# Kernel tuning notes

Measured on AMD Instinct MI355X. Metric: run time of the kernel, lower is better.

Reference implementation:

```python
import jax, jax.numpy as jnp
import numpy as np
import math

NUM_GROUPS = 8
NUM_HEADS = 4
EPS = 1e-5


def group_norm(x, gamma, beta):
    B, C, H, W = x.shape
    g = x.reshape(B, NUM_GROUPS, C // NUM_GROUPS, H, W)
    mean = g.mean(axis=(2, 3, 4), keepdims=True)
    var = g.var(axis=(2, 3, 4), keepdims=True)
    g = (g - mean) * jax.lax.rsqrt(var + EPS)
    x = g.reshape(B, C, H, W)
    return x * gamma[None, :, None, None] + beta[None, :, None, None]


def setup_inputs() -> dict:
    key = jax.random.key(0)
    ks = jax.random.split(key, 4)
    B, C, H, W = 4, 256, 64, 64
    x = jax.random.normal(ks[0], (B, C, H, W), dtype=jnp.float32)
    gamma = jnp.ones((C,), dtype=jnp.float32)
    beta = jnp.zeros((C,), dtype=jnp.float32)
    w_qkv = jax.random.normal(ks[1], (3 * C, C), dtype=jnp.float32) / math.sqrt(C)
    b_qkv = jnp.zeros((3 * C,), dtype=jnp.float32)
    w_proj = jax.random.normal(ks[2], (C, C), dtype=jnp.float32) / math.sqrt(C)
    b_proj = jnp.zeros((C,), dtype=jnp.float32)
    return {"x": x, "gamma": gamma, "beta": beta, "w_qkv": w_qkv,
            "b_qkv": b_qkv, "w_proj": w_proj, "b_proj": b_proj}


def reference(x, gamma, beta, w_qkv, b_qkv, w_proj, b_proj):
    B, C, H, W = x.shape
    hd = C // NUM_HEADS  # head dim
    h = group_norm(x, gamma, beta)
    # 1x1 conv == per-pixel matmul: [B,3C,H,W]
    qkv = jnp.einsum('bchw,oc->bohw', h, w_qkv) + b_qkv[None, :, None, None]
    q, k, v = jnp.split(qkv, 3, axis=1)

    def shape(t):
        # [B,C,H,W] -> [B, heads, HW, hd]
        return t.reshape(B, NUM_HEADS, hd, H * W).transpose(0, 1, 3, 2)

    q, k, v = shape(q), shape(k), shape(v)
    attn = jnp.einsum('bhqd,bhkd->bhqk', q, k) * (1.0 / math.sqrt(hd))
    attn = jax.nn.softmax(attn, axis=-1)
    out = jnp.einsum('bhqk,bhkd->bhqd', attn, v)
    # [B, heads, HW, hd] -> [B, C, H, W]
    out = out.transpose(0, 1, 3, 2).reshape(B, C, H, W)
    out = jnp.einsum('bchw,oc->bohw', out, w_proj) + b_proj[None, :, None, None]
    return x + out
```

## Files before the change

kernel.cpp:

```cpp
#include <hip/hip_runtime.h>
#include <math.h>

#define NB 4
#define C_ 256
#define NG 8
#define CPG 32
#define HW 4096
#define NH 4
#define HD 64
#define EPS 1e-5f
#define QSCALE 0.1803368801111204f

typedef __attribute__((ext_vector_type(8))) short bf16x8_t;
typedef __attribute__((ext_vector_type(4))) float f32x4_t;
typedef const __attribute__((address_space(1))) void g_void;
typedef __attribute__((address_space(3))) void l_void;

__device__ __forceinline__ unsigned short f2bf(float f) {
    unsigned u = __float_as_uint(f);
    u += 0x7FFFu + ((u >> 16) & 1u);
    return (unsigned short)(u >> 16);
}

__device__ __forceinline__ unsigned cvtpk(float lo, float hi) {
    unsigned r;
    asm("v_cvt_pk_bf16_f32 %0, %1, %2" : "=v"(r) : "v"(lo), "v"(hi));
    return r;
}

__device__ __forceinline__ void plswap16(unsigned &a, unsigned &b) {
#if __has_builtin(__builtin_amdgcn_permlane16_swap)
    auto r = __builtin_amdgcn_permlane16_swap(a, b, false, false);
    a = r[0]; b = r[1];
#else
    unsigned as = (unsigned)__shfl_xor((int)a, 16);
    unsigned bs = (unsigned)__shfl_xor((int)b, 16);
    bool hi = (threadIdx.x & 16) != 0;
    unsigned na = hi ? bs : a;
    unsigned nb = hi ? b : as;
    a = na; b = nb;
#endif
}
__device__ __forceinline__ void plswap32(unsigned &a, unsigned &b) {
#if __has_builtin(__builtin_amdgcn_permlane32_swap)
    auto r = __builtin_amdgcn_permlane32_swap(a, b, false, false);
    a = r[0]; b = r[1];
#else
    unsigned as = (unsigned)__shfl_xor((int)a, 32);
    unsigned bs = (unsigned)__shfl_xor((int)b, 32);
    bool hi = (threadIdx.x & 32) != 0;
    unsigned na = hi ? bs : a;
    unsigned nb = hi ? b : as;
    a = na; b = nb;
#endif
}

__global__ __launch_bounds__(256) void gn_stats_wconv_k(const float* __restrict__ x,
                                                        float2* __restrict__ part,
                                                        const float* __restrict__ wq,
                                                        const float* __restrict__ wp,
                                                        unsigned short* __restrict__ wt,
                                                        unsigned short* __restrict__ wpt) {
    if (blockIdx.x >= 1024) {
        int i4 = (blockIdx.x - 1024) * 256 + threadIdx.x;
        const float* src;
        unsigned short* dst;
        int off;
        if (i4 < 49152) { src = wq; dst = wt; off = i4 * 4; }
        else            { src = wp; dst = wpt; off = (i4 - 49152) * 4; }
        float4 v = *(const float4*)(src + off);
        ushort4 o;
        o.x = f2bf(v.x); o.y = f2bf(v.y); o.z = f2bf(v.z); o.w = f2bf(v.w);
        *(ushort4*)(dst + off) = o;
        return;
    }
    int bg = blockIdx.x >> 5, ch = blockIdx.x & 31;
    const float4* base = (const float4*)(x + (size_t)bg * CPG * HW + ch * 4096);
    float s = 0.f, ss = 0.f;
    #pragma unroll
    for (int i = threadIdx.x; i < 1024; i += 256) {
        float4 v = base[i];
        s  += v.x + v.y + v.z + v.w;
        ss += v.x*v.x + v.y*v.y + v.z*v.z + v.w*v.w;
    }
    #pragma unroll
    for (int off = 32; off > 0; off >>= 1) {
        s  += __shfl_down(s, off);
        ss += __shfl_down(ss, off);
    }
    __shared__ float rs[4], rss[4];
    int wv = threadIdx.x >> 6;
    if ((threadIdx.x & 63) == 0) { rs[wv] = s; rss[wv] = ss; }
    __syncthreads();
    if (threadIdx.x == 0)
        part[blockIdx.x] = make_float2(rs[0]+rs[1]+rs[2]+rs[3], rss[0]+rss[1]+rss[2]+rss[3]);
}

__global__ __launch_bounds__(256) void gn_apply_t_k(const float* __restrict__ x,
                                                    const float* __restrict__ gamma,
                                                    const float* __restrict__ beta,
                                                    const float2* __restrict__ part,
                                                    unsigned short* __restrict__ ht) {
    __shared__ unsigned short T[64 * 66];
    __shared__ float sstat[4];
    int b = blockIdx.z, c0 = blockIdx.y * 64, p0 = blockIdx.x * 64;
    int t = threadIdx.x;
    if (t < 64) {
        int half = t >> 5;
        int g = b * NG + (c0 >> 5) + half;
        float2 v = part[g * 32 + (t & 31)];
        float s = v.x, ss = v.y;
        #pragma unroll
        for (int off = 16; off > 0; off >>= 1) {
            s  += __shfl_xor(s, off);
            ss += __shfl_xor(ss, off);
        }
        if ((t & 31) == 0) {
            const float inv = 1.f / (float)(CPG * HW);
            float mean = s * inv;
            float var  = ss * inv - mean * mean;
            sstat[half * 2]     = mean;
            sstat[half * 2 + 1] = rsqrtf(var + EPS);
        }
    }
    __syncthreads();
    int cr = t >> 4, pc = t & 15;
    #pragma unroll
    for (int cp = 0; cp < 4; cp++) {
        int c = c0 + cp * 16 + cr;
        int gl = (cp * 16 + cr) >> 5;
        float mean = sstat[gl * 2], rstd = sstat[gl * 2 + 1];
        float sc = gamma[c] * rstd;
        float sh = beta[c] - mean * sc;
        float4 v = *(const float4*)(x + ((size_t)(b * C_ + c)) * HW + p0 + pc * 4);
        int cc = cp * 16 + cr;
        T[(pc*4 + 0) * 66 + cc] = f2bf(v.x*sc + sh);
        T[(pc*4 + 1) * 66 + cc] = f2bf(v.y*sc + sh);
        T[(pc*4 + 2) * 66 + cc] = f2bf(v.z*sc + sh);
        T[(pc*4 + 3) * 66 + cc] = f2bf(v.w*sc + sh);
    }
    __syncthreads();
    int p = t >> 2, cq = t & 3;
    const unsigned* rp = (const unsigned*)(T + p * 66 + cq * 16);
    unsigned short* dst = ht + ((size_t)b * HW + p0 + p) * 256 + c0 + cq * 16;
    *(uint4*)dst       = make_uint4(rp[0], rp[1], rp[2], rp[3]);
    *(uint4*)(dst + 8) = make_uint4(rp[4], rp[5], rp[6], rp[7]);
}

__global__ __launch_bounds__(256) void gemm_qkv_mfma_k(const unsigned short* __restrict__ wt,
                                                       const unsigned short* __restrict__ ht,
                                                       const float* __restrict__ bias,
                                                       unsigned short* __restrict__ qt,
                                                       unsigned short* __restrict__ kt,
                                                       unsigned short* __restrict__ vv) {
    __shared__ __align__(16) unsigned short smem[24576];
    int t = threadIdx.x, wave = t >> 6, lane = t & 63, quad = lane >> 4, l16 = lane & 15;
    int mq = wave & 1, pq = wave >> 1;
    int L = blockIdx.x;
    int W = (L & 7) * 96 + (L >> 3);
    int b = W / 192;
    int rem = W - b * 192;
    int px = rem / 6;
    int my = rem - px * 6;
    const char* Ag = (const char*)(wt + (size_t)(my * 128) * 256);
    const char* Bg = (const char*)(ht + ((size_t)b * HW + px * 128) * 256);

    int soff[2], lbs[2];
    #pragma unroll
    for (int n = 0; n < 2; n++) {
        int s = n * 256 + t;
        int row = s >> 2, c = (s & 3) ^ (row & 3);
        soff[n] = row * 512 + c * 16;
        lbs[n]  = s * 8;
    }

    auto STAGE = [&](int kc, int buf) {
        const char* a  = Ag + kc * 64;
        const char* bb = Bg + kc * 64;
        #pragma unroll
        for (int n = 0; n < 2; n++) {
            __builtin_amdgcn_global_load_lds((g_void*)(a  + soff[n]), (l_void*)(smem + buf * 8192 + lbs[n]), 16, 0, 0);
            __builtin_amdgcn_global_load_lds((g_void*)(bb + soff[n]), (l_void*)(smem + buf * 8192 + 4096 + lbs[n]), 16, 0, 0);
        }
    };

    f32x4_t acc[4][4];
    const f32x4_t zz = {0.f, 0.f, 0.f, 0.f};
    #pragma unroll
    for (int i = 0; i < 4; i++)
        #pragma unroll
        for (int j = 0; j < 4; j++) acc[i][j] = zz;

    STAGE(0, 0);
    STAGE(1, 1);
    int cur = 0;
    for (int kc = 0; kc < 8; kc++) {
        if (kc < 7) asm volatile("s_waitcnt vmcnt(4)" ::: "memory");
        else        asm volatile("s_waitcnt vmcnt(0)" ::: "memory");
        asm volatile("s_barrier" ::: "memory");
        if (kc + 2 < 8) { int nb = cur + 2; if (nb >= 3) nb -= 3; STAGE(kc + 2, nb); }
        const unsigned short* Ac = smem + cur * 8192;
        const unsigned short* Bc = smem + cur * 8192 + 4096;
        bf16x8_t af[4], bfr[4];
        #pragma unroll
        for (int mi = 0; mi < 4; mi++) {
            int R = mq * 64 + mi * 16 + l16;
            af[mi] = *(const bf16x8_t*)&Ac[(R * 4 + (quad ^ (R & 3))) * 8];
        }
        #pragma unroll
        for (int pi = 0; pi < 4; pi++) {
            int P = pq * 64 + pi * 16 + l16;
            bfr[pi] = *(const bf16x8_t*)&Bc[(P * 4 + (quad ^ (P & 3))) * 8];
        }
        __builtin_amdgcn_s_setprio(1);
        #pragma unroll
        for (int mi = 0; mi < 4; mi++)
            #pragma unroll
            for (int pi = 0; pi < 4; pi++)
                acc[mi][pi] = __builtin_amdgcn_mfma_f32_16x16x32_bf16(af[mi], bfr[pi], acc[mi][pi], 0, 0, 0);
        __builtin_amdgcn_s_setprio(0);
        cur = (cur + 1 == 3) ? 0 : cur + 1;
    }

    int sec = my >> 1;
    int hh = ((my & 1) << 1) | mq;
    if (sec < 2) {
        float scl = (sec == 0) ? QSCALE : 1.f;
        unsigned short* dst = ((sec == 0) ? qt : kt) + (size_t)(b * NH + hh) * HW * 64;
        #pragma unroll
        for (int mi = 0; mi < 4; mi++) {
            int d0 = mi * 16 + quad * 4;
            int mg = my * 128 + mq * 64 + d0;
            #pragma unroll
            for (int pi = 0; pi < 4; pi++) {
                int p = px * 128 + pq * 64 + pi * 16 + l16;
                unsigned lo = cvtpk((acc[mi][pi][0] + bias[mg + 0]) * scl,
                                    (acc[mi][pi][1] + bias[mg + 1]) * scl);
                unsigned hi = cvtpk((acc[mi][pi][2] + bias[mg + 2]) * scl,
                                    (acc[mi][pi][3] + bias[mg + 3]) * scl);
                *(uint2*)(dst + (size_t)p * 64 + d0) = make_uint2(lo, hi);
            }
        }
    } else {
        __syncthreads();
        unsigned short* T = smem;
        #pragma unroll
        for (int mi = 0; mi < 4; mi++) {
            int dT = mq * 64 + mi * 16 + quad * 4;
            int mg = my * 128 + dT;
            #pragma unroll
            for (int pi = 0; pi < 4; pi++) {
                int pl = pq * 64 + pi * 16 + l16;
                #pragma unroll
                for (int r = 0; r < 4; r++)
                    T[(dT + r) * 130 + pl] = f2bf(acc[mi][pi][r] + bias[mg + r]);
            }
        }
        __syncthreads();
        int dT = t >> 1, half = t & 1;
        const unsigned* rp = (const unsigned*)(T + dT * 130 + half * 64);
        unsigned short* dd = vv + ((size_t)(b * 256 + (my & 1) * 128 + dT)) * HW + px * 128 + half * 64;
        #pragma unroll
        for (int q8 = 0; q8 < 8; q8++)
            *(uint4*)(dd + q8 * 8) = make_uint4(rp[q8*4+0], rp[q8*4+1], rp[q8*4+2], rp[q8*4+3]);
    }
}

__global__ __launch_bounds__(256) void gemm_proj_mfma_k(const unsigned short* __restrict__ wpt,
                                                        const unsigned short* __restrict__ ao,
                                                        const float* __restrict__ bias,
                                                        const float* __restrict__ x,
                                                        float* __restrict__ out) {
    int b = blockIdx.z, my = blockIdx.y, px = blockIdx.x;
    int t = threadIdx.x, wave = t >> 6, lane = t & 63, quad = lane >> 4, l16 = lane & 15;
    int mw = wave & 1, pw = wave >> 1;
    const unsigned short* Ab = wpt + (size_t)(my * 64 + mw * 32) * 256;
    const unsigned short* Bb = ao + ((size_t)b * HW + px * 64 + pw * 32) * 256;
    f32x4_t acc[2][2];
    const f32x4_t zz = {0.f, 0.f, 0.f, 0.f};
    acc[0][0] = zz; acc[0][1] = zz; acc[1][0] = zz; acc[1][1] = zz;
    #pragma unroll
    for (int kc = 0; kc < 8; kc++) {
        bf16x8_t af[2], bfr[2];
        #pragma unroll
        for (int mi = 0; mi < 2; mi++)
            af[mi] = *(const bf16x8_t*)(Ab + (mi*16 + l16) * 256 + kc*32 + quad*8);
        #pragma unroll
        for (int pi = 0; pi < 2; pi++)
            bfr[pi] = *(const bf16x8_t*)(Bb + (size_t)(pi*16 + l16) * 256 + kc*32 + quad*8);
        #pragma unroll
        for (int mi = 0; mi < 2; mi++)
            #pragma unroll
            for (int pi = 0; pi < 2; pi++)
                acc[mi][pi] = __builtin_amdgcn_mfma_f32_16x16x32_bf16(af[mi], bfr[pi], acc[mi][pi], 0, 0, 0);
    }
    #pragma unroll
    for (int mi = 0; mi < 2; mi++)
        #pragma unroll
        for (int pi = 0; pi < 2; pi++) {
            int p = px*64 + pw*32 + pi*16 + l16;
            #pragma unroll
            for (int r = 0; r < 4; r++) {
                int m = my*64 + mw*32 + mi*16 + quad*4 + r;
                size_t off = (size_t)(b * C_ + m) * HW + p;
                out[off] = acc[mi][pi][r] + bias[m] + x[off];
            }
        }
}

__global__ __launch_bounds__(512) __attribute__((amdgpu_waves_per_eu(2, 8)))
void attn_k(const unsigned short* __restrict__ qt,
            const unsigned short* __restrict__ kt,
            const unsigned short* __restrict__ vv,
            unsigned short* __restrict__ ao) {
    __shared__ __align__(16) unsigned short smem[24576];
    int t = threadIdx.x;
    int wave = t >> 6, lane = t & 63, quad = lane >> 4, l16 = lane & 15;
    int iw = wave & 3, jw = wave >> 2;
    int L = blockIdx.x;
    int W = (L & 7) * 64 + (L >> 3);
    int i0 = (W & 31) * 128;
    int hh = (W >> 5) & 3;
    int b  = W >> 7;
    const unsigned short* qb = qt + (size_t)(b * NH + hh) * HW * 64;
    const char* kbp = (const char*)(kt + (size_t)(b * NH + hh) * HW * 64);
    const char* vbp = (const char*)(vv + (size_t)(b * NH + hh) * 64 * HW);

    bf16x8_t qf[2][2];
    #pragma unroll
    for (int mi = 0; mi < 2; mi++)
        #pragma unroll
        for (int kc = 0; kc < 2; kc++)
            qf[mi][kc] = *(const bf16x8_t*)(qb + (size_t)(i0 + iw * 32 + mi * 16 + l16) * 64 + kc * 32 + quad * 8);

    f32x4_t oacc[4][2], osum[2];
    const f32x4_t zz = {0.f, 0.f, 0.f, 0.f};
    #pragma unroll
    for (int dt = 0; dt < 4; dt++) { oacc[dt][0] = zz; oacc[dt][1] = zz; }
    osum[0] = zz; osum[1] = zz;

    bf16x8_t ones;
    #pragma unroll
    for (int e = 0; e < 8; e++) ones[e] = (short)0x3F80;

    bool isK = (jw == 0);
    int soff[2], lbase[2];
    #pragma unroll
    for (int n = 0; n < 2; n++) {
        int s = (iw * 2 + n) * 64 + lane;
        int row = s >> 3;
        int c = (s & 7) ^ (row & 7);
        soff[n] = isK ? (row * 128 + c * 16) : (row * (HW * 2) + c * 16);
        lbase[n] = (isK ? 0 : 12288) + (iw * 2 + n) * 512;
    }
    const char* gsrc0 = isK ? kbp : vbp;
    int tstride = isK ? 8192 : 128;

    auto STAGE = [&](int tile, int buf) {
        const char* g = gsrc0 + (size_t)tile * tstride;
        #pragma unroll
        for (int n = 0; n < 2; n++)
            __builtin_amdgcn_global_load_lds((g_void*)(g + soff[n]),
                                             (l_void*)(smem + buf * 4096 + lbase[n]), 16, 0, 0);
    };

    STAGE(0, 0);
    STAGE(1, 1);

    int cur = 0;
    for (int jt = 0; jt < 64; jt++) {
        if (jt < 63) asm volatile("s_waitcnt vmcnt(2)" ::: "memory");
        else         asm volatile("s_waitcnt vmcnt(0)" ::: "memory");
        asm volatile("s_barrier" ::: "memory");
        if (jt + 2 < 64) {
            int nb = cur + 2; if (nb >= 3) nb -= 3;
            STAGE(jt + 2, nb);
        }
        const unsigned short* Kc = smem + cur * 4096;
        const unsigned short* Vc = smem + 12288 + cur * 4096;

        f32x4_t sacc[2][2];
        sacc[0][0] = zz; sacc[0][1] = zz; sacc[1][0] = zz; sacc[1][1] = zz;
        __builtin_amdgcn_s_setprio(1);
        #pragma unroll
        for (int nj = 0; nj < 2; nj++) {
            int j = jw * 32 + nj * 16 + l16;
            int rb = j * 8;
            bf16x8_t kf0 = *(const bf16x8_t*)&Kc[(rb + ((quad    ) ^ (j & 7))) * 8];
            bf16x8_t kf1 = *(const bf16x8_t*)&Kc[(rb + ((4 + quad) ^ (j & 7))) * 8];
            #pragma unroll
            for (int mi = 0; mi < 2; mi++) {
                sacc[mi][nj] = __builtin_amdgcn_mfma_f32_16x16x32_bf16(kf0, qf[mi][0], sacc[mi][nj], 0, 0, 0);
                sacc[mi][nj] = __builtin_amdgcn_mfma_f32_16x16x32_bf16(kf1, qf[mi][1], sacc[mi][nj], 0, 0, 0);
            }
        }
        __builtin_amdgcn_s_setprio(0);

        bf16x8_t pf[2];
        #pragma unroll
        for (int mi = 0; mi < 2; mi++) {
            #pragma unroll
            for (int nj = 0; nj < 2; nj++)
                #pragma unroll
                for (int r = 0; r < 4; r++)
                    sacc[mi][nj][r] = __builtin_amdgcn_exp2f(sacc[mi][nj][r]);

            unsigned lo0 = cvtpk(sacc[mi][0][0], sacc[mi][0][1]);
            unsigned hi0 = cvtpk(sacc[mi][0][2], sacc[mi][0][3]);
            unsigned lo1 = cvtpk(sacc[mi][1][0], sacc[mi][1][1]);
            unsigned hi1 = cvtpk(sacc[mi][1][2], sacc[mi][1][3]);
            plswap32(lo0, lo1); plswap16(lo0, lo1);
            plswap32(hi0, hi1); plswap16(hi0, hi1);
            union { unsigned u[4]; bf16x8_t v8; } pu;
            pu.u[0] = lo0; pu.u[1] = hi0; pu.u[2] = lo1; pu.u[3] = hi1;
            pf[mi] = pu.v8;
        }

        __builtin_amdgcn_s_setprio(1);
        #pragma unroll
        for (int dt = 0; dt < 4; dt++) {
            int d = dt * 16 + l16;
            bf16x8_t vf = *(const bf16x8_t*)&Vc[(d * 8 + ((jw * 4 + quad) ^ (d & 7))) * 8];
            oacc[dt][0] = __builtin_amdgcn_mfma_f32_16x16x32_bf16(vf, pf[0], oacc[dt][0], 0, 0, 0);
            oacc[dt][1] = __builtin_amdgcn_mfma_f32_16x16x32_bf16(vf, pf[1], oacc[dt][1], 0, 0, 0);
        }
        osum[0] = __builtin_amdgcn_mfma_f32_16x16x32_bf16(ones, pf[0], osum[0], 0, 0, 0);
        osum[1] = __builtin_amdgcn_mfma_f32_16x16x32_bf16(ones, pf[1], osum[1], 0, 0, 0);
        __builtin_amdgcn_s_setprio(0);

        cur = (cur + 1 == 3) ? 0 : cur + 1;
    }

    __syncthreads();
    float* Obuf = (float*)smem;
    if (jw == 1) {
        #pragma unroll
        for (int mi = 0; mi < 2; mi++) {
            int R = iw * 32 + mi * 16 + l16;
            #pragma unroll
            for (int dt = 0; dt < 4; dt++)
                *(f32x4_t*)&Obuf[R * 68 + dt * 16 + quad * 4] = oacc[dt][mi];
            if (quad == 0)
                Obuf[R * 68 + 64] = osum[mi][0];
        }
    }
    __syncthreads();
    if (jw == 0) {
        #pragma unroll
        for (int mi = 0; mi < 2; mi++) {
            int R = iw * 32 + mi * 16 + l16;
            float l  = osum[mi][0] + Obuf[R * 68 + 64];
            float c0 = 1.f / l;
            unsigned short* dst = ao + ((size_t)b * HW + i0 + R) * 256 + hh * 64 + quad * 4;
            #pragma unroll
            for (int dt = 0; dt < 4; dt++) {
                f32x4_t o1 = *(const f32x4_t*)&Obuf[R * 68 + dt * 16 + quad * 4];
                unsigned w0 = cvtpk((oacc[dt][mi][0] + o1[0]) * c0,
                                    (oacc[dt][mi][1] + o1[1]) * c0);
                unsigned w1 = cvtpk((oacc[dt][mi][2] + o1[2]) * c0,
                                    (oacc[dt][mi][3] + o1[3]) * c0);
                *(uint2*)(dst + dt * 16) = make_uint2(w0, w1);
            }
        }
    }
}

extern "C" void kernel_launch(void* const* d_in, const int* in_sizes, int n_in,
                              void* d_out, int out_size, void* d_ws, size_t ws_size,
                              hipStream_t stream) {
    const float* x      = (const float*)d_in[0];
    const float* gamma  = (const float*)d_in[1];
    const float* beta   = (const float*)d_in[2];
    const float* w_qkv  = (const float*)d_in[3];
    const float* b_qkv  = (const float*)d_in[4];
    const float* w_proj = (const float*)d_in[5];
    const float* b_proj = (const float*)d_in[6];
    float* out = (float*)d_out;

    float* stats = (float*)d_ws;
    float2* part = (float2*)(stats + 256);
    unsigned short* ht  = (unsigned short*)(stats + 256 + 2048);
    unsigned short* qt  = ht + (size_t)4194304;
    unsigned short* kt  = qt + (size_t)4194304;
    unsigned short* vv  = kt + (size_t)4194304;
    unsigned short* ao  = vv + (size_t)4194304;
    unsigned short* wt  = ao + (size_t)4194304;
    unsigned short* wpt = wt + 196608;

    gn_stats_wconv_k<<<1280, 256, 0, stream>>>(x, part, w_qkv, w_proj, wt, wpt);
    gn_apply_t_k<<<dim3(64, 4, NB), 256, 0, stream>>>(x, gamma, beta, part, ht);
    gemm_qkv_mfma_k<<<768, 256, 0, stream>>>(wt, ht, b_qkv, qt, kt, vv);
    attn_k<<<512, 512, 0, stream>>>(qt, kt, vv, ao);
    gemm_proj_mfma_k<<<dim3(64, 4, NB), 256, 0, stream>>>(wpt, ao, b_proj, x, out);
}
```

Baseline: 190.5 us.

## Stage projection GEMM tiles through LDS with async triple buffering

The output projection GEMM now uses larger 128x128 tiles per block. Operands are staged into swizzled LDS through async global_load_lds with a three-buffer pipeline, replacing direct per-wave global fragment loads. The grid is flattened to 256 blocks with an interleaved block-to-tile mapping, and MFMA priority is raised during compute. This aims to improve operand reuse and overlap loads with MFMA, at the cost of fewer blocks and more LDS per block.

Result: faster. 182.2 us (median of 2 runs) (-4.4%).

```diff
diff --git a/kernel.cpp b/kernel.cpp
--- a/kernel.cpp
+++ b/kernel.cpp
@@ -271,37 +271,83 @@
                                                         const float* __restrict__ bias,
                                                         const float* __restrict__ x,
                                                         float* __restrict__ out) {
-    int b = blockIdx.z, my = blockIdx.y, px = blockIdx.x;
+    __shared__ __align__(16) unsigned short smem[24576];
     int t = threadIdx.x, wave = t >> 6, lane = t & 63, quad = lane >> 4, l16 = lane & 15;
-    int mw = wave & 1, pw = wave >> 1;
-    const unsigned short* Ab = wpt + (size_t)(my * 64 + mw * 32) * 256;
-    const unsigned short* Bb = ao + ((size_t)b * HW + px * 64 + pw * 32) * 256;
-    f32x4_t acc[2][2];
+    int mq = wave & 1, pq = wave >> 1;
+    int L = blockIdx.x;
+    int W = (L & 7) * 32 + (L >> 3);
+    int b = W >> 6;
+    int rem = W & 63;
+    int px = rem >> 1;
+    int my = rem & 1;
+    const char* Ag = (const char*)(wpt + (size_t)(my * 128) * 256);
+    const char* Bg = (const char*)(ao + ((size_t)b * HW + px * 128) * 256);
+
+    int soff[2], lbs[2];
+    #pragma unroll
+    for (int n = 0; n < 2; n++) {
+        int s = n * 256 + t;
+        int row = s >> 2, c = (s & 3) ^ (row & 3);
+        soff[n] = row * 512 + c * 16;
+        lbs[n]  = s * 8;
+    }
+
+    auto STAGE = [&](int kc, int buf) {
+        const char* a  = Ag + kc * 64;
+        const char* bb = Bg + kc * 64;
+        #pragma unroll
+        for (int n = 0; n < 2; n++) {
+            __builtin_amdgcn_global_load_lds((g_void*)(a  + soff[n]), (l_void*)(smem + buf * 8192 + lbs[n]), 16, 0, 0);
+            __builtin_amdgcn_global_load_lds((g_void*)(bb + soff[n]), (l_void*)(smem + buf * 8192 + 4096 + lbs[n]), 16, 0, 0);
+        }
+    };
+
+    f32x4_t acc[4][4];
     const f32x4_t zz = {0.f, 0.f, 0.f, 0.f};
-    acc[0][0] = zz; acc[0][1] = zz; acc[1][0] = zz; acc[1][1] = zz;
-    #pragma unroll
+    #pragma unroll
+    for (int i = 0; i < 4; i++)
+        #pragma unroll
+        for (int j = 0; j < 4; j++) acc[i][j] = zz;
+
+    STAGE(0, 0);
+    STAGE(1, 1);
+    int cur = 0;
     for (int kc = 0; kc < 8; kc++) {
-        bf16x8_t af[2], bfr[2];
-        #pragma unroll
-        for (int mi = 0; mi < 2; mi++)
-            af[mi] = *(const bf16x8_t*)(Ab + (mi*16 + l16) * 256 + kc*32 + quad*8);
-        #pragma unroll
-        for (int pi = 0; pi < 2; pi++)
-            bfr[pi] = *(const bf16x8_t*)(Bb + (size_t)(pi*16 + l16) * 256 + kc*32 + quad*8);
-        #pragma unroll
-        for (int mi = 0; mi < 2; mi++)
-            #pragma unroll
-            for (int pi = 0; pi < 2; pi++)
+        if (kc < 7) asm volatile("s_waitcnt vmcnt(4)" ::: "memory");
+        else        asm volatile("s_waitcnt vmcnt(0)" ::: "memory");
+        asm volatile("s_barrier" ::: "memory");
+        if (kc + 2 < 8) { int nb = cur + 2; if (nb >= 3) nb -= 3; STAGE(kc + 2, nb); }
+        const unsigned short* Ac = smem + cur * 8192;
+        const unsigned short* Bc = smem + cur * 8192 + 4096;
+        bf16x8_t af[4], bfr[4];
+        #pragma unroll
+        for (int mi = 0; mi < 4; mi++) {
+            int R = mq * 64 + mi * 16 + l16;
+            af[mi] = *(const bf16x8_t*)&Ac[(R * 4 + (quad ^ (R & 3))) * 8];
+        }
+        #pragma unroll
+        for (int pi = 0; pi < 4; pi++) {
+            int P = pq * 64 + pi * 16 + l16;
+            bfr[pi] = *(const bf16x8_t*)&Bc[(P * 4 + (quad ^ (P & 3))) * 8];
+        }
+        __builtin_amdgcn_s_setprio(1);
+        #pragma unroll
+        for (int mi = 0; mi < 4; mi++)
+            #pragma unroll
+            for (int pi = 0; pi < 4; pi++)
                 acc[mi][pi] = __builtin_amdgcn_mfma_f32_16x16x32_bf16(af[mi], bfr[pi], acc[mi][pi], 0, 0, 0);
-    }
-    #pragma unroll
-    for (int mi = 0; mi < 2; mi++)
-        #pragma unroll
-        for (int pi = 0; pi < 2; pi++) {
-            int p = px*64 + pw*32 + pi*16 + l16;
+        __builtin_amdgcn_s_setprio(0);
+        cur = (cur + 1 == 3) ? 0 : cur + 1;
+    }
+
+    #pragma unroll
+    for (int mi = 0; mi < 4; mi++)
+        #pragma unroll
+        for (int pi = 0; pi < 4; pi++) {
+            int p = px * 128 + pq * 64 + pi * 16 + l16;
             #pragma unroll
             for (int r = 0; r < 4; r++) {
-                int m = my*64 + mw*32 + mi*16 + quad*4 + r;
+                int m = my * 128 + mq * 64 + mi * 16 + quad * 4 + r;
                 size_t off = (size_t)(b * C_ + m) * HW + p;
                 out[off] = acc[mi][pi][r] + bias[m] + x[off];
             }
@@ -491,5 +537,5 @@
     gn_apply_t_k<<<dim3(64, 4, NB), 256, 0, stream>>>(x, gamma, beta, part, ht);
     gemm_qkv_mfma_k<<<768, 256, 0, stream>>>(wt, ht, b_qkv, qt, kt, vv);
     attn_k<<<512, 512, 0, stream>>>(qt, kt, vv, ao);
-    gemm_proj_mfma_k<<<dim3(64, 4, NB), 256, 0, stream>>>(wpt, ao, b_proj, x, out);
-}
+    gemm_proj_mfma_k<<<256, 256, 0, stream>>>(wpt, ao, b_proj, x, out);
+}
```
